# Optimization experiments

Hardware: AMD Instinct MI355X
Metric: run time of the kernel (lower is better)

The kernel has to match this reference:

```python
import jax, jax.numpy as jnp
import numpy as np

NEG_SLOPE = 0.2  # PyG GATConv default


def gat_layer(x, src, dst, W, a_src, a_dst, b, heads, ch, num_nodes):
    # x: [N, F_in]; W: [F_in, heads*ch]; a_src/a_dst: [heads, ch]; b: [heads*ch]
    h = (x @ W).reshape(num_nodes, heads, ch)                      # [N,H,C]
    al_s = jnp.einsum('nhc,hc->nh', h, a_src)                      # [N,H]
    al_d = jnp.einsum('nhc,hc->nh', h, a_dst)                      # [N,H]
    e = jax.nn.leaky_relu(al_s[src] + al_d[dst], NEG_SLOPE)        # [E,H]
    # segment softmax over incoming edges of each destination node
    emax = jax.ops.segment_max(e, dst, num_segments=num_nodes)     # [N,H]
    ee = jnp.exp(e - emax[dst])
    denom = jax.ops.segment_sum(ee, dst, num_segments=num_nodes)   # [N,H]
    alpha = ee / denom[dst]                                        # [E,H]
    msg = h[src] * alpha[..., None]                                # [E,H,C]
    out = jax.ops.segment_sum(msg, dst, num_segments=num_nodes)    # [N,H,C]
    return out.reshape(num_nodes, heads * ch) + b


def setup_inputs() -> dict:
    key = jax.random.key(0)
    ks = jax.random.split(key, 12)
    N, F_in, H1, C1, OUT = 50000, 128, 6, 32, 2
    E = 800000
    x = jax.random.normal(ks[0], (N, F_in), dtype=jnp.float32)
    edge_index = jax.random.randint(ks[1], (2, E), 0, N, dtype=jnp.int64)
    s = 0.1
    return {
        'x': x,
        'edge_index': edge_index,
        'W1': jax.random.normal(ks[2], (F_in, H1 * C1), dtype=jnp.float32) * s,
        'a1_src': jax.random.normal(ks[3], (H1, C1), dtype=jnp.float32) * s,
        'a1_dst': jax.random.normal(ks[4], (H1, C1), dtype=jnp.float32) * s,
        'b1': jnp.zeros((H1 * C1,), dtype=jnp.float32),
        'W2': jax.random.normal(ks[5], (H1 * C1, 1 * OUT), dtype=jnp.float32) * s,
        'a2_src': jax.random.normal(ks[6], (1, OUT), dtype=jnp.float32) * s,
        'a2_dst': jax.random.normal(ks[7], (1, OUT), dtype=jnp.float32) * s,
        'b2': jnp.zeros((OUT,), dtype=jnp.float32),
    }


def reference(x, edge_index, W1, a1_src, a1_dst, b1, W2, a2_src, a2_dst, b2):
    N = x.shape[0]
    loop = jnp.arange(N, dtype=edge_index.dtype)
    src = jnp.concatenate([edge_index[0], loop])  # add_self_loops=True (PyG default)
    dst = jnp.concatenate([edge_index[1], loop])
    h = gat_layer(x, src, dst, W1, a1_src, a1_dst, b1, heads=6, ch=32, num_nodes=N)
    h = jax.nn.relu(h)
    h = gat_layer(h, src, dst, W2, a2_src, a2_dst, b2, heads=1, ch=2, num_nodes=N)
    return jax.nn.log_softmax(h, axis=1)
```

## Files before the change

kernel.cpp:

```cpp
#include <hip/hip_runtime.h>
#include <hip/hip_fp16.h>

#define LRELU(v) ((v) > 0.0f ? (v) : 0.2f * (v))

constexpr int F_IN = 128;
constexpr int NH1  = 6;
constexpr int D1   = 192;

typedef _Float16 half8 __attribute__((ext_vector_type(8)));
typedef _Float16 half4v __attribute__((ext_vector_type(4)));
typedef float floatx4 __attribute__((ext_vector_type(4)));

__device__ __forceinline__ void wave_lds_fence() {
  __builtin_amdgcn_wave_barrier();
  asm volatile("s_waitcnt lgkmcnt(0)" ::: "memory");
  __builtin_amdgcn_wave_barrier();
}

__global__ __launch_bounds__(256) void k_hist(const float* __restrict__ W1,
                                              __half* __restrict__ w1t,
                                              const int* __restrict__ dst,
                                              int* __restrict__ cnt,
                                              int* __restrict__ pose, int E) {
  int tid = blockIdx.x * 256 + threadIdx.x;
  if (tid < F_IN * D1) {
    int k = tid / D1, n = tid - k * D1;
    w1t[(size_t)n * F_IN + k] = __float2half(W1[tid]);
  }
  if (tid < E) {
    pose[tid] = atomicAdd(&cnt[dst[tid]], 1);
  }
}

__global__ void k_scanA(const int* __restrict__ cnt, int* __restrict__ offs,
                        int* __restrict__ bsum, int N) {
  int t = threadIdx.x;
  int idx = blockIdx.x * 256 + t;
  int lane = t & 63, w = t >> 6;
  int v = (idx < N) ? cnt[idx] : 0;
  int incl = v;
#pragma unroll
  for (int d = 1; d < 64; d <<= 1) {
    int u = __shfl_up(incl, d);
    if (lane >= d) incl += u;
  }
  __shared__ int wt[4];
  if (lane == 63) wt[w] = incl;
  __syncthreads();
  int woff = 0;
  for (int i = 0; i < w; ++i) woff += wt[i];
  if (idx < N) offs[idx] = woff + incl - v;
  if (t == 255) bsum[blockIdx.x] = woff + incl;
}

__global__ __launch_bounds__(256) void k_scanC2(int* __restrict__ offs,
                                                const int* __restrict__ bsum,
                                                int N, int NB) {
  __shared__ int sh[2];
  int t = threadIdx.x;
  if (t < 64) {
    int pre = 0, tot = 0;
#pragma unroll
    for (int r = 0; r < 4; ++r) {
      int i = r * 64 + t;
      int b = (i < NB) ? bsum[i] : 0;
      if (i < (int)blockIdx.x) pre += b;
      tot += b;
    }
#pragma unroll
    for (int m = 32; m; m >>= 1) {
      pre += __shfl_xor(pre, m);
      tot += __shfl_xor(tot, m);
    }
    if (t == 0) { sh[0] = pre; sh[1] = tot; }
  }
  __syncthreads();
  int idx = blockIdx.x * 256 + t;
  if (idx < N) offs[idx] += sh[0];
  if (idx == 0) offs[N] = sh[1];
}

__global__ __launch_bounds__(256) void k_gp(
    const float* __restrict__ x, const __half* __restrict__ w1t,
    const float* __restrict__ a1s, const float* __restrict__ a1d,
    __half* __restrict__ h1h, float* __restrict__ als, float* __restrict__ ald,
    const int* __restrict__ src, const int* __restrict__ dst,
    const int* __restrict__ offs, const int* __restrict__ pose,
    int* __restrict__ ssort, int N, int E, int GB) {
  if ((int)blockIdx.x >= GB) {
    int e = ((int)blockIdx.x - GB) * 256 + threadIdx.x;
    if (e < E) ssort[offs[dst[e]] + pose[e]] = src[e];
    return;
  }

  int wv = blockIdx.x * 4 + (threadIdx.x >> 6);
  int m0 = wv * 16;
  if (m0 >= N) return;
  int lane = threadIdx.x & 63;
  int ln15 = lane & 15, q = lane >> 4;

  float avs[12], avd[12];
#pragma unroll
  for (int f = 0; f < 12; ++f) {
    int idx = (f >> 1) * 32 + (f & 1) * 16 + ln15;
    avs[f] = a1s[idx];
    avd[f] = a1d[idx];
  }

  floatx4 acc[12];
#pragma unroll
  for (int f = 0; f < 12; ++f) acc[f] = (floatx4){0.f, 0.f, 0.f, 0.f};

  int arowi = m0 + ln15;
  if (arowi >= N) arowi = N - 1;
  const float* arow = x + (size_t)arowi * F_IN + q * 8;
#pragma unroll
  for (int kc = 0; kc < F_IN; kc += 32) {
    float4 u0 = *(const float4*)(arow + kc);
    float4 u1 = *(const float4*)(arow + kc + 4);
    half8 a;
    a[0] = (_Float16)u0.x; a[1] = (_Float16)u0.y; a[2] = (_Float16)u0.z; a[3] = (_Float16)u0.w;
    a[4] = (_Float16)u1.x; a[5] = (_Float16)u1.y; a[6] = (_Float16)u1.z; a[7] = (_Float16)u1.w;
#pragma unroll
    for (int f = 0; f < 12; ++f) {
      half8 b = *(const half8*)(w1t + (size_t)(16 * f + ln15) * F_IN + kc + q * 8);
      acc[f] = __builtin_amdgcn_mfma_f32_16x16x32_f16(a, b, acc[f], 0, 0, 0);
    }
  }

#pragma unroll
  for (int f = 0; f < 12; ++f) {
#pragma unroll
    for (int r = 0; r < 4; ++r) {
      int n = m0 + q * 4 + r;
      if (n < N) h1h[(size_t)n * D1 + 16 * f + ln15] = __float2half(acc[f][r]);
    }
  }

#pragma unroll
  for (int r = 0; r < 4; ++r) {
    float ps[6] = {0.f, 0.f, 0.f, 0.f, 0.f, 0.f};
    float pd[6] = {0.f, 0.f, 0.f, 0.f, 0.f, 0.f};
#pragma unroll
    for (int f = 0; f < 12; ++f) {
      ps[f >> 1] = fmaf(acc[f][r], avs[f], ps[f >> 1]);
      pd[f >> 1] = fmaf(acc[f][r], avd[f], pd[f >> 1]);
    }
#pragma unroll
    for (int h = 0; h < 6; ++h) {
#pragma unroll
      for (int m = 8; m; m >>= 1) {
        ps[h] += __shfl_xor(ps[h], m);
        pd[h] += __shfl_xor(pd[h], m);
      }
    }
    float os = 0.f, od = 0.f;
#pragma unroll
    for (int h = 0; h < 6; ++h)
      if (ln15 == h) { os = ps[h]; od = pd[h]; }
    int n = m0 + q * 4 + r;
    if (ln15 < 6 && n < N) {
      als[(size_t)n * 6 + ln15] = os;
      ald[(size_t)n * 6 + ln15] = od;
    }
  }
}

__global__ __launch_bounds__(256) void k_agg1(
    const __half* __restrict__ h1h, const float* __restrict__ als, const float* __restrict__ ald,
    const int* __restrict__ offs, const int* __restrict__ srcs,
    const float* __restrict__ b1, const float* __restrict__ W2,
    const float* __restrict__ a2s, const float* __restrict__ a2d,
    float4* __restrict__ pk, int N) {
  __shared__ float wbuf[4][64][9];
  int wid = threadIdx.x >> 6, lane = threadIdx.x & 63;
  int d = blockIdx.x * 4 + wid;
  if (d >= N) return;
  int off = offs[d], cnt = offs[d + 1] - off;
  int tot = cnt + 1;

  float aldh[6];
  {
    const float* ap = ald + (size_t)d * 6;
    float2 q0 = *(const float2*)ap, q1 = *(const float2*)(ap + 2), q2 = *(const float2*)(ap + 4);
    aldh[0] = q0.x; aldh[1] = q0.y; aldh[2] = q1.x;
    aldh[3] = q1.y; aldh[4] = q2.x; aldh[5] = q2.y;
  }

  float dh[6] = {0.f, 0.f, 0.f, 0.f, 0.f, 0.f};
  int nchunk = (tot + 63) >> 6;

  const bool act = lane < 48;
  const int hd = lane >> 3;
  float a0 = 0.f, a1 = 0.f, a2 = 0.f, a3 = 0.f;

  auto body = [&](int j) {
    float w = wbuf[wid][j][hd < 6 ? hd : 0];
    int soff = __float_as_int(wbuf[wid][j][6]);
    const __half* hp = (const __half*)((const char*)h1h + soff);
    half4v v = *(const half4v*)(hp + 4 * lane);
    a0 = fmaf(w, (float)v[0], a0);
    a1 = fmaf(w, (float)v[1], a1);
    a2 = fmaf(w, (float)v[2], a2);
    a3 = fmaf(w, (float)v[3], a3);
  };
  auto jloop = [&](int jmax) {
    int j = 0;
    for (; j + 3 < jmax; j += 4) { body(j); body(j + 1); body(j + 2); body(j + 3); }
    for (; j < jmax; ++j) body(j);
  };

  if (nchunk == 1) {
    float wreg[6];
    int sreg = 0;
    if (lane < tot) {
      int s = (lane == cnt) ? d : srcs[off + lane];
      sreg = s;
      const float* ap = als + (size_t)s * 6;
      float2 p0 = *(const float2*)ap, p1 = *(const float2*)(ap + 2), p2 = *(const float2*)(ap + 4);
      float ev[6] = {p0.x, p0.y, p1.x, p1.y, p2.x, p2.y};
#pragma unroll
      for (int h = 0; h < 6; ++h) {
        float e = ev[h] + aldh[h];
        e = LRELU(e);
        wreg[h] = __expf(e);
        dh[h] = wreg[h];
      }
    }
#pragma unroll
    for (int h = 0; h < 6; ++h) {
#pragma unroll
      for (int m = 32; m; m >>= 1) dh[h] += __shfl_xor(dh[h], m);
      dh[h] = 1.0f / dh[h];
    }
    if (lane < tot) {
#pragma unroll
      for (int h = 0; h < 6; ++h) wbuf[wid][lane][h] = wreg[h] * dh[h];
      wbuf[wid][lane][6] = __int_as_float(sreg * (D1 * 2));
    }
    wave_lds_fence();
    if (act) jloop(tot);
  } else {
    for (int c = 0; c < nchunk; ++c) {
      int i = c * 64 + lane;
      if (i < tot) {
        int s = (i == cnt) ? d : srcs[off + i];
        const float* ap = als + (size_t)s * 6;
        float2 p0 = *(const float2*)ap, p1 = *(const float2*)(ap + 2), p2 = *(const float2*)(ap + 4);
        float ev[6] = {p0.x, p0.y, p1.x, p1.y, p2.x, p2.y};
#pragma unroll
        for (int h = 0; h < 6; ++h) {
          float e = ev[h] + aldh[h];
          e = LRELU(e);
          dh[h] += __expf(e);
        }
      }
    }
#pragma unroll
    for (int h = 0; h < 6; ++h) {
#pragma unroll
      for (int m = 32; m; m >>= 1) dh[h] += __shfl_xor(dh[h], m);
      dh[h] = 1.0f / dh[h];
    }
    for (int c = 0; c < nchunk; ++c) {
      int i = c * 64 + lane;
      if (i < tot) {
        int s = (i == cnt) ? d : srcs[off + i];
        const float* ap = als + (size_t)s * 6;
        float2 p0 = *(const float2*)ap, p1 = *(const float2*)(ap + 2), p2 = *(const float2*)(ap + 4);
        float ev[6] = {p0.x, p0.y, p1.x, p1.y, p2.x, p2.y};
#pragma unroll
        for (int h = 0; h < 6; ++h) {
          float e = ev[h] + aldh[h];
          e = LRELU(e);
          wbuf[wid][lane][h] = __expf(e) * dh[h];
        }
        wbuf[wid][lane][6] = __int_as_float(s * (D1 * 2));
      }
      wave_lds_fence();
      int jmax = tot - c * 64;
      if (jmax > 64) jmax = 64;
      if (act) jloop(jmax);
      wave_lds_fence();
    }
  }

  float s0 = 0.f, s1 = 0.f;
  if (act) {
    float4 bv = *(const float4*)(b1 + 4 * lane);
    float v0 = fmaxf(a0 + bv.x, 0.f);
    float v1 = fmaxf(a1 + bv.y, 0.f);
    float v2 = fmaxf(a2 + bv.z, 0.f);
    float v3 = fmaxf(a3 + bv.w, 0.f);
    float4 w01 = *(const float4*)(W2 + 8 * lane);
    float4 w23 = *(const float4*)(W2 + 8 * lane + 4);
    s0 = v0 * w01.x + v1 * w01.z + v2 * w23.x + v3 * w23.z;
    s1 = v0 * w01.y + v1 * w01.w + v2 * w23.y + v3 * w23.w;
  }
#pragma unroll
  for (int m = 32; m; m >>= 1) {
    s0 += __shfl_xor(s0, m);
    s1 += __shfl_xor(s1, m);
  }
  if (lane == 0) {
    pk[d] = make_float4(s0, s1,
                        s0 * a2s[0] + s1 * a2s[1],
                        s0 * a2d[0] + s1 * a2d[1]);
  }
}

__global__ __launch_bounds__(256) void k_agg2(
    const float4* __restrict__ pk, const int* __restrict__ offs,
    const int* __restrict__ srcs, const float* __restrict__ b2,
    float* __restrict__ out, int N) {
  int tid = blockIdx.x * 256 + threadIdx.x;
  int g = tid >> 3, r = tid & 7;
  if (g >= N) return;
  int off = offs[g], cnt = offs[g + 1] - off;
  int tot = cnt + 1;
  float ad = pk[g].w;
  float den = 0.f, o0 = 0.f, o1 = 0.f;
  for (int i = r; i < tot; i += 8) {
    int s = (i == cnt) ? g : srcs[off + i];
    float4 p = pk[s];
    float e = p.z + ad;
    e = LRELU(e);
    float a = __expf(e);
    den += a;
    o0 = fmaf(a, p.x, o0);
    o1 = fmaf(a, p.y, o1);
  }
#pragma unroll
  for (int m = 4; m; m >>= 1) {
    den += __shfl_xor(den, m);
    o0 += __shfl_xor(o0, m);
    o1 += __shfl_xor(o1, m);
  }
  if (r == 0) {
    float inv = 1.0f / den;
    o0 = o0 * inv + b2[0];
    o1 = o1 * inv + b2[1];
    float mm = fmaxf(o0, o1);
    float l = mm + logf(__expf(o0 - mm) + __expf(o1 - mm));
    *(float2*)(out + (size_t)g * 2) = make_float2(o0 - l, o1 - l);
  }
}

extern "C" void kernel_launch(void* const* d_in, const int* in_sizes, int n_in,
                              void* d_out, int out_size, void* d_ws, size_t ws_size,
                              hipStream_t stream) {
  const float* x   = (const float*)d_in[0];
  const int*   ei  = (const int*)d_in[1];
  const float* W1  = (const float*)d_in[2];
  const float* a1s = (const float*)d_in[3];
  const float* a1d = (const float*)d_in[4];
  const float* b1  = (const float*)d_in[5];
  const float* W2  = (const float*)d_in[6];
  const float* a2s = (const float*)d_in[7];
  const float* a2d = (const float*)d_in[8];
  const float* b2  = (const float*)d_in[9];
  float* out = (float*)d_out;

  const int N = in_sizes[0] / F_IN;
  const int E = in_sizes[1] / 2;
  const int* srcp = ei;
  const int* dstp = ei + E;

  char* w = (char*)d_ws;
  auto alloc = [&](size_t bytes) {
    char* p = w;
    w += (bytes + 255) & ~(size_t)255;
    return p;
  };
  __half* h1h   = (__half*)alloc((size_t)N * D1 * 2 + 256);
  __half* w1t   = (__half*)alloc((size_t)F_IN * D1 * 2);
  float* als    = (float*)alloc((size_t)N * NH1 * 4);
  float* ald    = (float*)alloc((size_t)N * NH1 * 4);
  float4* pk    = (float4*)alloc((size_t)N * 16);
  int*   cnt    = (int*)alloc((size_t)N * 4);
  int*   offs   = (int*)alloc((size_t)(N + 1) * 4);
  int*   pose   = (int*)alloc((size_t)E * 4);
  int*   ssort  = (int*)alloc((size_t)E * 4);
  int*   bsum   = (int*)alloc(1024);

  const int NB = (N + 255) / 256;
  const int GB = ((N + 15) / 16 + 3) / 4;
  const int PB = (E + 255) / 256;

  hipMemsetAsync(cnt, 0, (size_t)N * 4, stream);
  k_hist<<<(E + 255) / 256, 256, 0, stream>>>(W1, w1t, dstp, cnt, pose, E);
  k_scanA<<<NB, 256, 0, stream>>>(cnt, offs, bsum, N);
  k_scanC2<<<NB, 256, 0, stream>>>(offs, bsum, N, NB);
  k_gp<<<GB + PB, 256, 0, stream>>>(x, w1t, a1s, a1d, h1h, als, ald,
                                    srcp, dstp, offs, pose, ssort, N, E, GB);
  k_agg1<<<(N + 3) / 4, 256, 0, stream>>>(h1h, als, ald, offs, ssort, b1, W2,
                                          a2s, a2d, pk, N);
  k_agg2<<<(N * 8 + 255) / 256, 256, 0, stream>>>(pk, offs, ssort, b2, out, N);
}
```

Measured before the change: 225.4 us.

## Split layer-1 aggregation into eight column slices with padded h1 layout

The layer-1 aggregation now launches eight blocks per destination group, each handling a 24-column slice of the 192 features. Within a wave, 8 edges are processed in parallel and each edge gets 6 lanes. h1 is stored in a padded 256-half row layout so each slice's 48-byte segment is 64-byte aligned. Softmax normalisation is deferred to the end, so only the one or two heads a slice touches are computed per edge. A new k_fin kernel reduces the eight partial layer-2 projections. The aim is more parallelism and better lane utilisation on the gather, at the cost of recomputing edge weights and reloading indices eight times, plus an extra kernel and intermediate buffer.

```diff
diff --git a/kernel.cpp b/kernel.cpp
--- a/kernel.cpp
+++ b/kernel.cpp
@@ -6,6 +6,7 @@
 constexpr int F_IN = 128;
 constexpr int NH1  = 6;
 constexpr int D1   = 192;
+constexpr int RP   = 256;
 
 typedef _Float16 half8 __attribute__((ext_vector_type(8)));
 typedef _Float16 half4v __attribute__((ext_vector_type(4)));
@@ -83,7 +84,7 @@
 __global__ __launch_bounds__(256) void k_gp(
     const float* __restrict__ x, const __half* __restrict__ w1t,
     const float* __restrict__ a1s, const float* __restrict__ a1d,
-    __half* __restrict__ h1h, float* __restrict__ als, float* __restrict__ ald,
+    __half* __restrict__ h1p, float* __restrict__ als, float* __restrict__ ald,
     const int* __restrict__ src, const int* __restrict__ dst,
     const int* __restrict__ offs, const int* __restrict__ pose,
     int* __restrict__ ssort, int N, int E, int GB) {
@@ -130,10 +131,12 @@
 
 #pragma unroll
   for (int f = 0; f < 12; ++f) {
+    int c = 16 * f + ln15;
+    int pos = c + 8 * ((c * 2731) >> 16);
 #pragma unroll
     for (int r = 0; r < 4; ++r) {
       int n = m0 + q * 4 + r;
-      if (n < N) h1h[(size_t)n * D1 + 16 * f + ln15] = __float2half(acc[f][r]);
+      if (n < N) h1p[(size_t)n * RP + pos] = __float2half(acc[f][r]);
     }
   }
 
@@ -166,147 +169,123 @@
   }
 }
 
-__global__ __launch_bounds__(256) void k_agg1(
-    const __half* __restrict__ h1h, const float* __restrict__ als, const float* __restrict__ ald,
+__global__ __launch_bounds__(256) void k_agg1s(
+    const __half* __restrict__ h1p, const float* __restrict__ als, const float* __restrict__ ald,
     const int* __restrict__ offs, const int* __restrict__ srcs,
     const float* __restrict__ b1, const float* __restrict__ W2,
-    const float* __restrict__ a2s, const float* __restrict__ a2d,
-    float4* __restrict__ pk, int N) {
-  __shared__ float wbuf[4][64][9];
+    float2* __restrict__ pp, int N) {
+  __shared__ float wbuf[4][64][3];
   int wid = threadIdx.x >> 6, lane = threadIdx.x & 63;
-  int d = blockIdx.x * 4 + wid;
+  int L = blockIdx.x & 7;
+  int d = ((int)blockIdx.x >> 3) * 4 + wid;
   if (d >= N) return;
   int off = offs[d], cnt = offs[d + 1] - off;
   int tot = cnt + 1;
 
-  float aldh[6];
-  {
-    const float* ap = ald + (size_t)d * 6;
-    float2 q0 = *(const float2*)ap, q1 = *(const float2*)(ap + 2), q2 = *(const float2*)(ap + 4);
-    aldh[0] = q0.x; aldh[1] = q0.y; aldh[2] = q1.x;
-    aldh[3] = q1.y; aldh[4] = q2.x; aldh[5] = q2.y;
-  }
-
-  float dh[6] = {0.f, 0.f, 0.f, 0.f, 0.f, 0.f};
-  int nchunk = (tot + 63) >> 6;
-
-  const bool act = lane < 48;
-  const int hd = lane >> 3;
-  float a0 = 0.f, a1 = 0.f, a2 = 0.f, a3 = 0.f;
-
-  auto body = [&](int j) {
-    float w = wbuf[wid][j][hd < 6 ? hd : 0];
-    int soff = __float_as_int(wbuf[wid][j][6]);
-    const __half* hp = (const __half*)((const char*)h1h + soff);
-    half4v v = *(const half4v*)(hp + 4 * lane);
-    a0 = fmaf(w, (float)v[0], a0);
-    a1 = fmaf(w, (float)v[1], a1);
-    a2 = fmaf(w, (float)v[2], a2);
-    a3 = fmaf(w, (float)v[3], a3);
-  };
-  auto jloop = [&](int jmax) {
-    int j = 0;
-    for (; j + 3 < jmax; j += 4) { body(j); body(j + 1); body(j + 2); body(j + 3); }
-    for (; j < jmax; ++j) body(j);
-  };
-
-  if (nchunk == 1) {
-    float wreg[6];
-    int sreg = 0;
-    if (lane < tot) {
-      int s = (lane == cnt) ? d : srcs[off + lane];
-      sreg = s;
-      const float* ap = als + (size_t)s * 6;
-      float2 p0 = *(const float2*)ap, p1 = *(const float2*)(ap + 2), p2 = *(const float2*)(ap + 4);
-      float ev[6] = {p0.x, p0.y, p1.x, p1.y, p2.x, p2.y};
-#pragma unroll
-      for (int h = 0; h < 6; ++h) {
-        float e = ev[h] + aldh[h];
-        e = LRELU(e);
-        wreg[h] = __expf(e);
-        dh[h] = wreg[h];
+  const int c0 = 24 * L;
+  const int hlo = c0 >> 5;
+  const int hhi = (c0 + 23) >> 5;
+  const float ald_lo = ald[(size_t)d * 6 + hlo];
+  const float ald_hi = ald[(size_t)d * 6 + hhi];
+
+  const int g = lane >> 3, m = lane & 7;
+  const bool act = m < 6;
+  const int myc = c0 + 4 * m;
+  const int mysel = ((myc >> 5) != hlo) ? 1 : 0;
+  const int boff = 64 * L + 8 * m;
+
+  float acc0 = 0.f, acc1 = 0.f, acc2 = 0.f, acc3 = 0.f;
+  float den_lo = 0.f, den_hi = 0.f;
+
+  for (int base = 0; base < tot; base += 64) {
+    int i = base + lane;
+    if (i < tot) {
+      int s = (i == cnt) ? d : srcs[off + i];
+      float elo = als[(size_t)s * 6 + hlo] + ald_lo;
+      elo = LRELU(elo);
+      float wlo = __expf(elo);
+      float whi;
+      if (hhi != hlo) {
+        float ehi = als[(size_t)s * 6 + hhi] + ald_hi;
+        ehi = LRELU(ehi);
+        whi = __expf(ehi);
+      } else {
+        whi = wlo;
       }
-    }
-#pragma unroll
-    for (int h = 0; h < 6; ++h) {
-#pragma unroll
-      for (int m = 32; m; m >>= 1) dh[h] += __shfl_xor(dh[h], m);
-      dh[h] = 1.0f / dh[h];
-    }
-    if (lane < tot) {
-#pragma unroll
-      for (int h = 0; h < 6; ++h) wbuf[wid][lane][h] = wreg[h] * dh[h];
-      wbuf[wid][lane][6] = __int_as_float(sreg * (D1 * 2));
+      den_lo += wlo;
+      den_hi += whi;
+      wbuf[wid][lane][0] = wlo;
+      wbuf[wid][lane][1] = whi;
+      wbuf[wid][lane][2] = __int_as_float(s * (RP * 2));
     }
     wave_lds_fence();
-    if (act) jloop(tot);
-  } else {
-    for (int c = 0; c < nchunk; ++c) {
-      int i = c * 64 + lane;
-      if (i < tot) {
-        int s = (i == cnt) ? d : srcs[off + i];
-        const float* ap = als + (size_t)s * 6;
-        float2 p0 = *(const float2*)ap, p1 = *(const float2*)(ap + 2), p2 = *(const float2*)(ap + 4);
-        float ev[6] = {p0.x, p0.y, p1.x, p1.y, p2.x, p2.y};
-#pragma unroll
-        for (int h = 0; h < 6; ++h) {
-          float e = ev[h] + aldh[h];
-          e = LRELU(e);
-          dh[h] += __expf(e);
-        }
+    int jmax = tot - base;
+    if (jmax > 64) jmax = 64;
+    for (int j = 0; j < jmax; j += 8) {
+      int jg = j + g;
+      if (act && jg < jmax) {
+        float w = wbuf[wid][jg][mysel];
+        int soff = __float_as_int(wbuf[wid][jg][2]);
+        half4v v = *(const half4v*)((const char*)h1p + soff + boff);
+        acc0 = fmaf(w, (float)v[0], acc0);
+        acc1 = fmaf(w, (float)v[1], acc1);
+        acc2 = fmaf(w, (float)v[2], acc2);
+        acc3 = fmaf(w, (float)v[3], acc3);
       }
     }
-#pragma unroll
-    for (int h = 0; h < 6; ++h) {
-#pragma unroll
-      for (int m = 32; m; m >>= 1) dh[h] += __shfl_xor(dh[h], m);
-      dh[h] = 1.0f / dh[h];
-    }
-    for (int c = 0; c < nchunk; ++c) {
-      int i = c * 64 + lane;
-      if (i < tot) {
-        int s = (i == cnt) ? d : srcs[off + i];
-        const float* ap = als + (size_t)s * 6;
-        float2 p0 = *(const float2*)ap, p1 = *(const float2*)(ap + 2), p2 = *(const float2*)(ap + 4);
-        float ev[6] = {p0.x, p0.y, p1.x, p1.y, p2.x, p2.y};
-#pragma unroll
-        for (int h = 0; h < 6; ++h) {
-          float e = ev[h] + aldh[h];
-          e = LRELU(e);
-          wbuf[wid][lane][h] = __expf(e) * dh[h];
-        }
-        wbuf[wid][lane][6] = __int_as_float(s * (D1 * 2));
-      }
-      wave_lds_fence();
-      int jmax = tot - c * 64;
-      if (jmax > 64) jmax = 64;
-      if (act) jloop(jmax);
-      wave_lds_fence();
-    }
+    wave_lds_fence();
+  }
+
+#pragma unroll
+  for (int mm = 32; mm; mm >>= 1) {
+    den_lo += __shfl_xor(den_lo, mm);
+    den_hi += __shfl_xor(den_hi, mm);
+  }
+#pragma unroll
+  for (int mm = 8; mm < 64; mm <<= 1) {
+    acc0 += __shfl_xor(acc0, mm);
+    acc1 += __shfl_xor(acc1, mm);
+    acc2 += __shfl_xor(acc2, mm);
+    acc3 += __shfl_xor(acc3, mm);
   }
 
   float s0 = 0.f, s1 = 0.f;
-  if (act) {
-    float4 bv = *(const float4*)(b1 + 4 * lane);
-    float v0 = fmaxf(a0 + bv.x, 0.f);
-    float v1 = fmaxf(a1 + bv.y, 0.f);
-    float v2 = fmaxf(a2 + bv.z, 0.f);
-    float v3 = fmaxf(a3 + bv.w, 0.f);
-    float4 w01 = *(const float4*)(W2 + 8 * lane);
-    float4 w23 = *(const float4*)(W2 + 8 * lane + 4);
+  if (act && g == 0) {
+    float dinv = 1.0f / (mysel ? den_hi : den_lo);
+    float4 bv = *(const float4*)(b1 + myc);
+    float v0 = fmaxf(acc0 * dinv + bv.x, 0.f);
+    float v1 = fmaxf(acc1 * dinv + bv.y, 0.f);
+    float v2 = fmaxf(acc2 * dinv + bv.z, 0.f);
+    float v3 = fmaxf(acc3 * dinv + bv.w, 0.f);
+    float4 w01 = *(const float4*)(W2 + 2 * myc);
+    float4 w23 = *(const float4*)(W2 + 2 * myc + 4);
     s0 = v0 * w01.x + v1 * w01.z + v2 * w23.x + v3 * w23.z;
     s1 = v0 * w01.y + v1 * w01.w + v2 * w23.y + v3 * w23.w;
   }
 #pragma unroll
-  for (int m = 32; m; m >>= 1) {
-    s0 += __shfl_xor(s0, m);
-    s1 += __shfl_xor(s1, m);
-  }
-  if (lane == 0) {
-    pk[d] = make_float4(s0, s1,
-                        s0 * a2s[0] + s1 * a2s[1],
-                        s0 * a2d[0] + s1 * a2d[1]);
-  }
+  for (int mm = 32; mm; mm >>= 1) {
+    s0 += __shfl_xor(s0, mm);
+    s1 += __shfl_xor(s1, mm);
+  }
+  if (lane == 0) pp[(size_t)d * 8 + L] = make_float2(s0, s1);
+}
+
+__global__ __launch_bounds__(256) void k_fin(const float2* __restrict__ pp,
+                                             const float* __restrict__ a2s,
+                                             const float* __restrict__ a2d,
+                                             float4* __restrict__ pk, int N) {
+  int d = blockIdx.x * 256 + threadIdx.x;
+  if (d >= N) return;
+  float s0 = 0.f, s1 = 0.f;
+#pragma unroll
+  for (int l = 0; l < 8; ++l) {
+    float2 p = pp[(size_t)d * 8 + l];
+    s0 += p.x;
+    s1 += p.y;
+  }
+  pk[d] = make_float4(s0, s1,
+                      s0 * a2s[0] + s1 * a2s[1],
+                      s0 * a2d[0] + s1 * a2d[1]);
 }
 
 __global__ __launch_bounds__(256) void k_agg2(
@@ -372,10 +351,11 @@
     w += (bytes + 255) & ~(size_t)255;
     return p;
   };
-  __half* h1h   = (__half*)alloc((size_t)N * D1 * 2 + 256);
+  __half* h1p   = (__half*)alloc((size_t)N * RP * 2);
   __half* w1t   = (__half*)alloc((size_t)F_IN * D1 * 2);
   float* als    = (float*)alloc((size_t)N * NH1 * 4);
   float* ald    = (float*)alloc((size_t)N * NH1 * 4);
+  float2* pp    = (float2*)alloc((size_t)N * 8 * 8);
   float4* pk    = (float4*)alloc((size_t)N * 16);
   int*   cnt    = (int*)alloc((size_t)N * 4);
   int*   offs   = (int*)alloc((size_t)(N + 1) * 4);
@@ -386,14 +366,15 @@
   const int NB = (N + 255) / 256;
   const int GB = ((N + 15) / 16 + 3) / 4;
   const int PB = (E + 255) / 256;
+  const int AB = ((N + 3) / 4) * 8;
 
   hipMemsetAsync(cnt, 0, (size_t)N * 4, stream);
   k_hist<<<(E + 255) / 256, 256, 0, stream>>>(W1, w1t, dstp, cnt, pose, E);
   k_scanA<<<NB, 256, 0, stream>>>(cnt, offs, bsum, N);
   k_scanC2<<<NB, 256, 0, stream>>>(offs, bsum, N, NB);
-  k_gp<<<GB + PB, 256, 0, stream>>>(x, w1t, a1s, a1d, h1h, als, ald,
+  k_gp<<<GB + PB, 256, 0, stream>>>(x, w1t, a1s, a1d, h1p, als, ald,
                                     srcp, dstp, offs, pose, ssort, N, E, GB);
-  k_agg1<<<(N + 3) / 4, 256, 0, stream>>>(h1h, als, ald, offs, ssort, b1, W2,
-                                          a2s, a2d, pk, N);
+  k_agg1s<<<AB, 256, 0, stream>>>(h1p, als, ald, offs, ssort, b1, W2, pp, N);
+  k_fin<<<NB, 256, 0, stream>>>(pp, a2s, a2d, pk, N);
   k_agg2<<<(N * 8 + 255) / 256, 256, 0, stream>>>(pk, offs, ssort, b2, out, N);
 }
```

Result: slower. 386.6 us (+71.6%).
